# Performance work log

Measured on AMD Instinct MI355X. Metric: run time of the kernel, lower is better.

The kernel has to match this reference:

```python
import jax, jax.numpy as jnp
import numpy as np

ISIZE = 1024
OSIZE = 1024
EPS = 1e-5  # torch nn.LayerNorm default


def setup_inputs() -> dict:
    key = jax.random.key(0)
    k0, k1, k2 = jax.random.split(key, 3)
    B, S = 32, 256
    x = jax.random.normal(k0, (B, S, ISIZE), dtype=jnp.float32)
    # Linear(isize + osize, 4*osize): W stored as (in, out) for x @ W
    scale = 1.0 / np.sqrt(ISIZE + OSIZE)
    W = jax.random.uniform(k1, (ISIZE + OSIZE, 4 * OSIZE), dtype=jnp.float32,
                           minval=-scale, maxval=scale)
    b = jax.random.uniform(k2, (4 * OSIZE,), dtype=jnp.float32,
                           minval=-scale, maxval=scale)
    gamma = jnp.ones((4, OSIZE), dtype=jnp.float32)   # LayerNorm((4, osize)) weight
    beta = jnp.zeros((4, OSIZE), dtype=jnp.float32)   # LayerNorm((4, osize)) bias
    init_hx = jnp.zeros((1, OSIZE), dtype=jnp.float32)
    init_cx = jnp.zeros((1, OSIZE), dtype=jnp.float32)
    return {"x": x, "W": W, "b": b, "gamma": gamma, "beta": beta,
            "init_hx": init_hx, "init_cx": init_cx}


def _layernorm_2d(z, gamma, beta):
    # Normalize jointly over the last two dims (4, osize), per torch LayerNorm((4, osize))
    mean = jnp.mean(z, axis=(-2, -1), keepdims=True)
    var = jnp.var(z, axis=(-2, -1), keepdims=True)
    return (z - mean) * jax.lax.rsqrt(var + EPS) * gamma + beta


def reference(x, W, b, gamma, beta, init_hx, init_cx):
    B, S, _ = x.shape
    osize = init_hx.shape[-1]
    hx = jnp.broadcast_to(init_hx, (B, osize))  # prepare_initState: expand to batch
    cx = jnp.broadcast_to(init_cx, (B, osize))

    def step(carry, xt):
        h, c = carry
        comb = jnp.concatenate([xt, h], axis=-1) @ W + b       # [B, 4*osize]
        comb = _layernorm_2d(comb.reshape(B, 4, osize), gamma, beta)
        ig, fg, hidden, og = comb[:, 0], comb[:, 1], comb[:, 2], comb[:, 3]
        c = jax.nn.sigmoid(fg) * c + jax.nn.sigmoid(ig) * jnp.tanh(hidden)
        h = jax.nn.sigmoid(og) * c                              # RNMT+ cell: out = og * cell
        return (h, c), h

    xs = jnp.swapaxes(x, 0, 1)                                  # [S, B, isize]
    _, outs = jax.lax.scan(step, (hx, cx), xs)
    return jnp.swapaxes(outs, 0, 1)                             # [B, S, osize]
```

## Files before the change

kernel.cpp:

```cpp
#include <hip/hip_runtime.h>
#include <hip/hip_bf16.h>

#define NB 32
#define NS 256
#define NI 1024
#define NO 1024
#define NK 2048
#define NC 4096
#define LN_EPS 1e-5f

typedef __attribute__((ext_vector_type(4))) float f32x4;
typedef __attribute__((ext_vector_type(4))) unsigned int u32x4;

__device__ __forceinline__ f32x4 mfma_bf16_16x16x32(u32x4 a, u32x4 b, f32x4 c) {
  asm volatile("v_mfma_f32_16x16x32_bf16 %0, %1, %2, %0" : "+v"(c) : "v"(a), "v"(b));
  return c;
}

__device__ __forceinline__ float sigf(float x) { return 1.0f / (1.0f + __expf(-x)); }
__device__ __forceinline__ float tanhfast(float x) {
  return 1.0f - 2.0f / (__expf(2.0f * x) + 1.0f);
}


__global__ void pack_x(const float* __restrict__ x, __hip_bfloat16* __restrict__ xfrag) {
  const int t = blockIdx.x, kt = blockIdx.y;
  const int tid = threadIdx.x;
  const int plane = tid >> 6, l = tid & 63, q = (l >> 4), ln = l & 15;
  const int m = plane * 16 + ln;
  const float* src = x + ((size_t)m * NS + t) * NI + kt * 32 + q * 8;
  float4 v0 = *(const float4*)src;
  float4 v1 = *(const float4*)(src + 4);
  __align__(16) __hip_bfloat16 tmp[8];
  tmp[0] = __float2bfloat16(v0.x); tmp[1] = __float2bfloat16(v0.y);
  tmp[2] = __float2bfloat16(v0.z); tmp[3] = __float2bfloat16(v0.w);
  tmp[4] = __float2bfloat16(v1.x); tmp[5] = __float2bfloat16(v1.y);
  tmp[6] = __float2bfloat16(v1.z); tmp[7] = __float2bfloat16(v1.w);
  *(u32x4*)(xfrag + (((size_t)t * 32 + kt) * 2 + plane) * 512 + l * 8) = *(const u32x4*)tmp;
}

__global__ void pack_wf(const float* __restrict__ W, __hip_bfloat16* __restrict__ WF) {
  const int blk = blockIdx.x;
  const int b = blk >> 6, kt = blk & 63;
  const int l = threadIdx.x, q = l >> 4, c = l & 15;
  const int n  = ((c >> 2) << 10) + b * 4 + (c & 3);
  const int k0 = kt * 32 + q * 8;
  __align__(16) __hip_bfloat16 tmp[8];
#pragma unroll
  for (int j = 0; j < 8; ++j)
    tmp[j] = __float2bfloat16(W[(size_t)(k0 + j) * NC + n]);
  *(u32x4*)(WF + ((size_t)(b * 64 + kt) * 64 + l) * 8) = *(const u32x4*)tmp;
}

__device__ __forceinline__ size_t hfrag_idx(int m, int j) {
  const int kt = j >> 5, q = (j >> 3) & 3, jj = j & 7;
  const int plane = m >> 4, l = q * 16 + (m & 15);
  return (((size_t)kt * 2 + plane) * 64 + l) * 8 + jj;
}

__global__ void init_state(const float* __restrict__ hx0, const float* __restrict__ cx0,
                           __hip_bfloat16* __restrict__ hfrag, float* __restrict__ cst,
                           float* __restrict__ hf) {
  const int i = blockIdx.x * 256 + threadIdx.x;
  const int m = i >> 10, j = i & (NO - 1);
  const float hv = hx0[j];
  hfrag[hfrag_idx(m, j)] = __float2bfloat16(hv);
  hf[i]  = hv;
  cst[i] = cx0[j];
}

__global__ __launch_bounds__(512)
void xgemm_all(const __hip_bfloat16* __restrict__ xfrag,
               const __hip_bfloat16* __restrict__ WF,
               const float* __restrict__ bias,
               __hip_bfloat16* __restrict__ xa) {
  __shared__ __align__(16) float xch[8 * 2 * 256];
  const int b = blockIdx.x, tid = threadIdx.x;
  const int wv = tid >> 6, l = tid & 63;
  const int kt0 = wv * 4;
  u32x4 bb[4];
  {
    const __hip_bfloat16* bp = WF + ((size_t)(b * 64 + kt0) * 64 + l) * 8;
#pragma unroll
    for (int i = 0; i < 4; ++i) bb[i] = *(const u32x4*)(bp + (size_t)i * 512);
  }
  const int row = tid >> 4, c = tid & 15;
  const int p = row >> 4, rr = row & 15;
  const int idx = ((rr >> 2) * 16 + c) * 4 + (rr & 3);
  const int n = ((c >> 2) << 10) + b * 4 + (c & 3);
  const float bn = bias[n];

  for (int t = 0; t < NS; ++t) {
    f32x4 acc0 = {0.f, 0.f, 0.f, 0.f}, acc1 = {0.f, 0.f, 0.f, 0.f};
    asm volatile("s_nop 1" ::);
    const __hip_bfloat16* ap = xfrag + ((size_t)t * 32 + kt0) * 1024 + l * 8;
#pragma unroll
    for (int i = 0; i < 4; ++i) {
      u32x4 a0 = *(const u32x4*)(ap + (size_t)i * 1024);
      u32x4 a1 = *(const u32x4*)(ap + (size_t)i * 1024 + 512);
      acc0 = mfma_bf16_16x16x32(a0, bb[i], acc0);
      acc1 = mfma_bf16_16x16x32(a1, bb[i], acc1);
    }
    asm volatile("s_nop 7\n\ts_nop 7" ::);
    *(f32x4*)(xch + (wv * 2 + 0) * 256 + l * 4) = acc0;
    *(f32x4*)(xch + (wv * 2 + 1) * 256 + l * 4) = acc1;
    __syncthreads();
    float v = bn;
#pragma unroll
    for (int w = 0; w < 8; ++w) v += xch[(w * 2 + p) * 256 + idx];
    xa[((size_t)t * 256 + b) * 512 + tid] = __float2bfloat16(v);
    __syncthreads();
  }
}

__global__ __launch_bounds__(512)
void step_gemm_h(const __hip_bfloat16* __restrict__ hfrag,
                 const __hip_bfloat16* __restrict__ WF,
                 const __hip_bfloat16* __restrict__ xa,
                 float* __restrict__ comb, int t) {
  __shared__ __align__(16) float xch[8 * 2 * 256];
  const int b = blockIdx.x, tid = threadIdx.x;
  const int wv = tid >> 6, l = tid & 63;
  const int kt0 = wv * 4;
  const __hip_bfloat16* ap = hfrag + (size_t)kt0 * 1024 + l * 8;
  const __hip_bfloat16* bp = WF + ((size_t)(b * 64 + 32 + kt0) * 64 + l) * 8;

  f32x4 acc0 = {0.f, 0.f, 0.f, 0.f}, acc1 = {0.f, 0.f, 0.f, 0.f};
  asm volatile("s_nop 1" ::);
#pragma unroll
  for (int i = 0; i < 4; ++i) {
    u32x4 a0 = *(const u32x4*)(ap + (size_t)i * 1024);
    u32x4 a1 = *(const u32x4*)(ap + (size_t)i * 1024 + 512);
    u32x4 bbv = *(const u32x4*)(bp + (size_t)i * 512);
    acc0 = mfma_bf16_16x16x32(a0, bbv, acc0);
    acc1 = mfma_bf16_16x16x32(a1, bbv, acc1);
  }
  asm volatile("s_nop 7\n\ts_nop 7" ::);

  *(f32x4*)(xch + (wv * 2 + 0) * 256 + l * 4) = acc0;
  *(f32x4*)(xch + (wv * 2 + 1) * 256 + l * 4) = acc1;
  __syncthreads();

  const int row = tid >> 4, c = tid & 15;
  const int p = row >> 4, rr = row & 15;
  const int idx = ((rr >> 2) * 16 + c) * 4 + (rr & 3);
  const int n = ((c >> 2) << 10) + b * 4 + (c & 3);
  float v = __bfloat162float(xa[((size_t)t * 256 + b) * 512 + tid]);
#pragma unroll
  for (int w = 0; w < 8; ++w) v += xch[(w * 2 + p) * 256 + idx];
  comb[(size_t)row * NC + n] = v;
}

__global__ __launch_bounds__(512)
void step_gemm_mfma(const __hip_bfloat16* __restrict__ xfrag,
                    const __hip_bfloat16* __restrict__ hfrag,
                    const __hip_bfloat16* __restrict__ WF,
                    const float* __restrict__ bias,
                    float* __restrict__ comb, int t) {
  __shared__ __align__(16) float xch[8 * 2 * 256];
  const int b = blockIdx.x, tid = threadIdx.x;
  const int wv = tid >> 6, l = tid & 63;

  const __hip_bfloat16* ap = (wv < 4)
      ? xfrag + ((size_t)t * 32 + wv * 8) * 1024 + l * 8
      : hfrag + ((size_t)(wv - 4) * 8) * 1024 + l * 8;
  const __hip_bfloat16* bp = WF + ((size_t)(b * 64 + wv * 8) * 64 + l) * 8;

  f32x4 acc0 = {0.f, 0.f, 0.f, 0.f}, acc1 = {0.f, 0.f, 0.f, 0.f};
  asm volatile("s_nop 1" ::);
#pragma unroll
  for (int i = 0; i < 8; ++i) {
    u32x4 a0 = *(const u32x4*)(ap + (size_t)i * 1024);
    u32x4 a1 = *(const u32x4*)(ap + (size_t)i * 1024 + 512);
    u32x4 bb = *(const u32x4*)(bp + (size_t)i * 512);
    acc0 = mfma_bf16_16x16x32(a0, bb, acc0);
    acc1 = mfma_bf16_16x16x32(a1, bb, acc1);
  }
  asm volatile("s_nop 7\n\ts_nop 7" ::);

  *(f32x4*)(xch + (wv * 2 + 0) * 256 + l * 4) = acc0;
  *(f32x4*)(xch + (wv * 2 + 1) * 256 + l * 4) = acc1;
  __syncthreads();

  const int row = tid >> 4, c = tid & 15;
  const int p = row >> 4, rr = row & 15;
  const int idx = ((rr >> 2) * 16 + c) * 4 + (rr & 3);
  const int n = ((c >> 2) << 10) + b * 4 + (c & 3);
  float v = bias[n];
#pragma unroll
  for (int w = 0; w < 8; ++w) v += xch[(w * 2 + p) * 256 + idx];
  comb[(size_t)row * NC + n] = v;
}

__global__ __launch_bounds__(1024)
void step_update_row(const float* __restrict__ comb,
                     const float* __restrict__ gamma,
                     const float* __restrict__ beta,
                     float* __restrict__ cst,
                     float* __restrict__ out,
                     __hip_bfloat16* __restrict__ hfrag,
                     int t) {
  __shared__ __align__(16) float combL[NC];
  __shared__ float red[16][2];
  __shared__ float stat[2];
  const int m = blockIdx.x, tid = threadIdx.x;

  f32x4 cv = *(const f32x4*)(comb + (size_t)m * NC + tid * 4);
  *(f32x4*)(combL + tid * 4) = cv;
  float s  = cv[0] + cv[1] + cv[2] + cv[3];
  float ss = cv[0] * cv[0] + cv[1] * cv[1] + cv[2] * cv[2] + cv[3] * cv[3];
#pragma unroll
  for (int off = 1; off < 64; off <<= 1) {
    s  += __shfl_xor(s, off);
    ss += __shfl_xor(ss, off);
  }
  const int wid = tid >> 6;
  if ((tid & 63) == 0) { red[wid][0] = s; red[wid][1] = ss; }
  __syncthreads();
  if (tid == 0) {
    float s2 = 0.f, ss2 = 0.f;
#pragma unroll
    for (int i = 0; i < 16; ++i) { s2 += red[i][0]; ss2 += red[i][1]; }
    const float mean = s2 * (1.f / NC);
    const float var  = ss2 * (1.f / NC) - mean * mean;
    stat[0] = mean;
    stat[1] = rsqrtf(var + LN_EPS);
  }
  __syncthreads();
  const float mean = stat[0], rs = stat[1];
  const int j = tid;
  const float iv = (combL[j]          - mean) * rs * gamma[j]          + beta[j];
  const float fv = (combL[NO + j]     - mean) * rs * gamma[NO + j]     + beta[NO + j];
  const float gv = (combL[2 * NO + j] - mean) * rs * gamma[2 * NO + j] + beta[2 * NO + j];
  const float ov = (combL[3 * NO + j] - mean) * rs * gamma[3 * NO + j] + beta[3 * NO + j];
  const float cold = cst[(size_t)m * NO + j];
  const float cc = sigf(fv) * cold + sigf(iv) * tanhfast(gv);
  const float hh = sigf(ov) * cc;
  cst[(size_t)m * NO + j] = cc;
  out[((size_t)m * NS + t) * NO + j] = hh;
  hfrag[hfrag_idx(m, j)] = __float2bfloat16(hh);
}


__launch_bounds__(256)
__global__ void step_gemm_f32(const float* __restrict__ x, const float* __restrict__ hf,
                              const float* __restrict__ W, const float* __restrict__ bias,
                              float* __restrict__ comb, int t) {
  const int blk = blockIdx.x;
  const int tid = threadIdx.x;
  const int n   = blk * 16 + (tid & 15);
  const int mlo = tid >> 4;
  float a0 = 0.f, a1 = 0.f;
  for (int k = 0; k < NI; ++k) {
    const float wv = W[(size_t)k * NC + n];
    a0 += x[((size_t)mlo * NS + t) * NI + k] * wv;
    a1 += x[((size_t)(mlo + 16) * NS + t) * NI + k] * wv;
  }
  for (int k = 0; k < NO; ++k) {
    const float wv = W[(size_t)(NI + k) * NC + n];
    a0 += hf[mlo * NO + k] * wv;
    a1 += hf[(mlo + 16) * NO + k] * wv;
  }
  comb[(size_t)mlo * NC + n] = a0 + bias[n];
  comb[(size_t)(mlo + 16) * NC + n] = a1 + bias[n];
}

__global__ __launch_bounds__(1024)
void step_update_row_f32(const float* __restrict__ comb,
                         const float* __restrict__ gamma,
                         const float* __restrict__ beta,
                         float* __restrict__ cst,
                         float* __restrict__ out,
                         float* __restrict__ hf,
                         int t) {
  __shared__ __align__(16) float combL[NC];
  __shared__ float red[16][2];
  __shared__ float stat[2];
  const int m = blockIdx.x, tid = threadIdx.x;
  f32x4 cv = *(const f32x4*)(comb + (size_t)m * NC + tid * 4);
  *(f32x4*)(combL + tid * 4) = cv;
  float s  = cv[0] + cv[1] + cv[2] + cv[3];
  float ss = cv[0] * cv[0] + cv[1] * cv[1] + cv[2] * cv[2] + cv[3] * cv[3];
#pragma unroll
  for (int off = 1; off < 64; off <<= 1) {
    s  += __shfl_xor(s, off);
    ss += __shfl_xor(ss, off);
  }
  const int wid = tid >> 6;
  if ((tid & 63) == 0) { red[wid][0] = s; red[wid][1] = ss; }
  __syncthreads();
  if (tid == 0) {
    float s2 = 0.f, ss2 = 0.f;
    for (int i = 0; i < 16; ++i) { s2 += red[i][0]; ss2 += red[i][1]; }
    const float mean = s2 * (1.f / NC);
    const float var  = ss2 * (1.f / NC) - mean * mean;
    stat[0] = mean;
    stat[1] = rsqrtf(var + LN_EPS);
  }
  __syncthreads();
  const float mean = stat[0], rs = stat[1];
  const int j = tid;
  const float iv = (combL[j]          - mean) * rs * gamma[j]          + beta[j];
  const float fv = (combL[NO + j]     - mean) * rs * gamma[NO + j]     + beta[NO + j];
  const float gv = (combL[2 * NO + j] - mean) * rs * gamma[2 * NO + j] + beta[2 * NO + j];
  const float ov = (combL[3 * NO + j] - mean) * rs * gamma[3 * NO + j] + beta[3 * NO + j];
  const float cold = cst[(size_t)m * NO + j];
  const float cc = sigf(fv) * cold + sigf(iv) * tanhfast(gv);
  const float hh = sigf(ov) * cc;
  cst[(size_t)m * NO + j] = cc;
  out[((size_t)m * NS + t) * NO + j] = hh;
  hf[(size_t)m * NO + j] = hh;
}


extern "C" void kernel_launch(void* const* d_in, const int* in_sizes, int n_in,
                              void* d_out, int out_size, void* d_ws, size_t ws_size,
                              hipStream_t stream) {
  (void)in_sizes; (void)n_in; (void)out_size;
  const float* x     = (const float*)d_in[0];
  const float* W     = (const float*)d_in[1];
  const float* bias  = (const float*)d_in[2];
  const float* gamma = (const float*)d_in[3];
  const float* beta  = (const float*)d_in[4];
  const float* hx0   = (const float*)d_in[5];
  const float* cx0   = (const float*)d_in[6];
  float* outp = (float*)d_out;

  char* ws = (char*)d_ws;
  size_t off = 0;
  auto alloc = [&](size_t bytes) -> char* {
    off = (off + 255) & ~(size_t)255;
    char* p = ws + off;
    off += bytes;
    return p;
  };
  float* comb           = (float*)alloc((size_t)NB * NC * 4);
  float* cst            = (float*)alloc((size_t)NB * NO * 4);
  float* hf             = (float*)alloc((size_t)NB * NO * 4);
  __hip_bfloat16* hfrag = (__hip_bfloat16*)alloc((size_t)NB * NO * 2);
  __hip_bfloat16* xfrag = (__hip_bfloat16*)alloc((size_t)NB * NS * NI * 2);
  __hip_bfloat16* WF    = (__hip_bfloat16*)alloc((size_t)NK * NC * 2);
  const size_t off_tier2 = off;
  __hip_bfloat16* xa    = (__hip_bfloat16*)alloc((size_t)NS * NB * NC * 2);
  const size_t off_tier1 = off;

  const bool tier1 = (ws_size >= off_tier1);
  const bool tier2 = (ws_size >= off_tier2);

  if (tier1) {
    hipLaunchKernelGGL(init_state, dim3((NB * NO) / 256), dim3(256), 0, stream,
                       hx0, cx0, hfrag, cst, hf);
    hipLaunchKernelGGL(pack_x, dim3(NS, 32), dim3(128), 0, stream, x, xfrag);
    hipLaunchKernelGGL(pack_wf, dim3(256 * 64), dim3(64), 0, stream, W, WF);
    hipLaunchKernelGGL(xgemm_all, dim3(256), dim3(512), 0, stream,
                       xfrag, WF, bias, xa);
    for (int t = 0; t < NS; ++t) {
      hipLaunchKernelGGL(step_gemm_h, dim3(256), dim3(512), 0, stream,
                         hfrag, WF, xa, comb, t);
      hipLaunchKernelGGL(step_update_row, dim3(NB), dim3(1024), 0, stream,
                         comb, gamma, beta, cst, outp, hfrag, t);
    }
  } else if (tier2) {
    hipLaunchKernelGGL(init_state, dim3((NB * NO) / 256), dim3(256), 0, stream,
                       hx0, cx0, hfrag, cst, hf);
    hipLaunchKernelGGL(pack_x, dim3(NS, 32), dim3(128), 0, stream, x, xfrag);
    hipLaunchKernelGGL(pack_wf, dim3(256 * 64), dim3(64), 0, stream, W, WF);
    for (int t = 0; t < NS; ++t) {
      hipLaunchKernelGGL(step_gemm_mfma, dim3(256), dim3(512), 0, stream,
                         xfrag, hfrag, WF, bias, comb, t);
      hipLaunchKernelGGL(step_update_row, dim3(NB), dim3(1024), 0, stream,
                         comb, gamma, beta, cst, outp, hfrag, t);
    }
  } else {
    hipLaunchKernelGGL(init_state, dim3((NB * NO) / 256), dim3(256), 0, stream,
                       hx0, cx0, hfrag, cst, hf);
    for (int t = 0; t < NS; ++t) {
      hipLaunchKernelGGL(step_gemm_f32, dim3(256), dim3(256), 0, stream,
                         x, hf, W, bias, comb, t);
      hipLaunchKernelGGL(step_update_row_f32, dim3(NB), dim3(1024), 0, stream,
                         comb, gamma, beta, cst, outp, hf, t);
    }
  }
}
```

Before: 2.497 ms.

## Fuse per-step h-GEMM and LayerNorm/LSTM update via atomic grid barrier

Merges the per-timestep recurrent GEMM and the row-wise LayerNorm plus gate update into one kernel, so each step needs one launch instead of two. Row sum and sum-of-squares are accumulated with coherent float atomics into per-step slots. An atomic counter acts as a grid-wide barrier before each block normalises and updates its own columns. This removes a launch and the round trip of the comb buffer through global memory. In exchange it assumes all 256 blocks are co-resident, and it takes variance as E[x^2]-mean^2 in fp32, which is less numerically stable.

```diff
diff --git a/kernel.cpp b/kernel.cpp
--- a/kernel.cpp
+++ b/kernel.cpp
@@ -8,6 +8,10 @@
 #define NK 2048
 #define NC 4096
 #define LN_EPS 1e-5f
+#define SPIN_GUARD (1 << 18)
+
+#define SROW_STRIDE 16
+#define CNT_STRIDE  32
 
 typedef __attribute__((ext_vector_type(4))) float f32x4;
 typedef __attribute__((ext_vector_type(4))) unsigned int u32x4;
@@ -20,6 +24,30 @@
 __device__ __forceinline__ float sigf(float x) { return 1.0f / (1.0f + __expf(-x)); }
 __device__ __forceinline__ float tanhfast(float x) {
   return 1.0f - 2.0f / (__expf(2.0f * x) + 1.0f);
+}
+
+__device__ __forceinline__ unsigned int load_coh_u32(const void* p) {
+  unsigned int v;
+  asm volatile("global_load_dword %0, %1, off sc0 sc1\n\ts_waitcnt vmcnt(0)"
+               : "=&v"(v) : "v"(p));
+  return v;
+}
+#define COH_LOAD2_F32(d0, d1, a0, a1)                                   \
+  asm volatile("global_load_dword %0, %2, off sc0 sc1\n\t"              \
+               "global_load_dword %1, %3, off sc0 sc1\n\t"              \
+               "s_waitcnt vmcnt(0)"                                     \
+               : "=&v"(d0), "=&v"(d1) : "v"(a0), "v"(a1))
+__device__ __forceinline__ void atomic_add_coh_u32(void* p, unsigned int v) {
+  asm volatile("global_atomic_add %0, %1, off sc1" :: "v"(p), "v"(v) : "memory");
+}
+__device__ __forceinline__ void atomic_add_coh_f32(void* p, float v) {
+  asm volatile("global_atomic_add_f32 %0, %1, off sc1" :: "v"(p), "v"(v) : "memory");
+}
+__device__ __forceinline__ void poll_coh_ge(const unsigned int* p, unsigned int target) {
+  for (int g = 0; g < SPIN_GUARD; ++g) {
+    if (load_coh_u32(p) >= target) return;
+    __builtin_amdgcn_s_sleep(2);
+  }
 }
 
 
@@ -114,16 +142,25 @@
 }
 
 __global__ __launch_bounds__(512)
-void step_gemm_h(const __hip_bfloat16* __restrict__ hfrag,
-                 const __hip_bfloat16* __restrict__ WF,
-                 const __hip_bfloat16* __restrict__ xa,
-                 float* __restrict__ comb, int t) {
+void step_fused(__hip_bfloat16* hfrag,
+                const __hip_bfloat16* __restrict__ WF,
+                const __hip_bfloat16* __restrict__ xa,
+                const float* __restrict__ gamma,
+                const float* __restrict__ beta,
+                float* __restrict__ cst,
+                float* __restrict__ out,
+                float* __restrict__ srow_t,
+                unsigned int* __restrict__ scnt_t,
+                int t) {
   __shared__ __align__(16) float xch[8 * 2 * 256];
+  __shared__ __align__(16) float combB[32 * 16];
   const int b = blockIdx.x, tid = threadIdx.x;
   const int wv = tid >> 6, l = tid & 63;
+
   const int kt0 = wv * 4;
   const __hip_bfloat16* ap = hfrag + (size_t)kt0 * 1024 + l * 8;
   const __hip_bfloat16* bp = WF + ((size_t)(b * 64 + 32 + kt0) * 64 + l) * 8;
+  const float xav = __bfloat162float(xa[((size_t)t * 256 + b) * 512 + tid]);
 
   f32x4 acc0 = {0.f, 0.f, 0.f, 0.f}, acc1 = {0.f, 0.f, 0.f, 0.f};
   asm volatile("s_nop 1" ::);
@@ -142,13 +179,65 @@
   __syncthreads();
 
   const int row = tid >> 4, c = tid & 15;
-  const int p = row >> 4, rr = row & 15;
-  const int idx = ((rr >> 2) * 16 + c) * 4 + (rr & 3);
-  const int n = ((c >> 2) << 10) + b * 4 + (c & 3);
-  float v = __bfloat162float(xa[((size_t)t * 256 + b) * 512 + tid]);
-#pragma unroll
-  for (int w = 0; w < 8; ++w) v += xch[(w * 2 + p) * 256 + idx];
-  comb[(size_t)row * NC + n] = v;
+  {
+    const int p = row >> 4, rr = row & 15;
+    const int idx = ((rr >> 2) * 16 + c) * 4 + (rr & 3);
+    float v = xav;
+#pragma unroll
+    for (int w = 0; w < 8; ++w) v += xch[(w * 2 + p) * 256 + idx];
+    combB[row * 16 + c] = v;
+    float s = v, ss = v * v;
+#pragma unroll
+    for (int off = 1; off < 16; off <<= 1) {
+      s  += __shfl_xor(s, off);
+      ss += __shfl_xor(ss, off);
+    }
+    if (c == 0) {
+      float* slot = srow_t + row * SROW_STRIDE;
+      atomic_add_coh_f32(slot + 0, s);
+      atomic_add_coh_f32(slot + 8, ss);
+    }
+  }
+  asm volatile("s_waitcnt vmcnt(0)" ::: "memory");
+  __syncthreads();
+  if (tid == 0) {
+    atomic_add_coh_u32(scnt_t, 1u);
+    poll_coh_ge(scnt_t, 256u);
+  }
+  __syncthreads();
+
+  if (wv == 0) {
+    const int gm = l >> 1, gh = l & 1;
+    const int j0 = b * 4 + 2 * gh;
+    const float* slot = srow_t + gm * SROW_STRIDE;
+    float sv, ssv;
+    COH_LOAD2_F32(sv, ssv, slot + 0, slot + 8);
+    const float mean = sv * (1.f / NC);
+    const float var  = ssv * (1.f / NC) - mean * mean;
+    const float rs = rsqrtf(var + LN_EPS);
+    const int cb = 2 * gh;
+    float pre[4][2];
+#pragma unroll
+    for (int g = 0; g < 4; ++g) {
+      const float ga0 = gamma[g * NO + j0], ga1 = gamma[g * NO + j0 + 1];
+      const float be0 = beta[g * NO + j0],  be1 = beta[g * NO + j0 + 1];
+      pre[g][0] = (combB[gm * 16 + g * 4 + cb]     - mean) * rs * ga0 + be0;
+      pre[g][1] = (combB[gm * 16 + g * 4 + cb + 1] - mean) * rs * ga1 + be1;
+    }
+    float2 cold = *(const float2*)(cst + (size_t)gm * NO + j0);
+    const float cc0 = sigf(pre[1][0]) * cold.x + sigf(pre[0][0]) * tanhfast(pre[2][0]);
+    const float cc1 = sigf(pre[1][1]) * cold.y + sigf(pre[0][1]) * tanhfast(pre[2][1]);
+    const float hh0 = sigf(pre[3][0]) * cc0;
+    const float hh1 = sigf(pre[3][1]) * cc1;
+    float2 cnew; cnew.x = cc0; cnew.y = cc1;
+    *(float2*)(cst + (size_t)gm * NO + j0) = cnew;
+    float2 o2; o2.x = hh0; o2.y = hh1;
+    *(float2*)(out + ((size_t)gm * NS + t) * NO + j0) = o2;
+    __hip_bfloat16 hb0 = __float2bfloat16(hh0), hb1 = __float2bfloat16(hh1);
+    unsigned int hp = (unsigned int)*(unsigned short*)&hb0 |
+                      ((unsigned int)*(unsigned short*)&hb1 << 16);
+    *(unsigned int*)(hfrag + hfrag_idx(gm, j0)) = hp;
+  }
 }
 
 __global__ __launch_bounds__(512)
@@ -338,6 +427,8 @@
   float* cst            = (float*)alloc((size_t)NB * NO * 4);
   float* hf             = (float*)alloc((size_t)NB * NO * 4);
   __hip_bfloat16* hfrag = (__hip_bfloat16*)alloc((size_t)NB * NO * 2);
+  float* srow           = (float*)alloc((size_t)NS * 32 * SROW_STRIDE * 4);
+  unsigned int* scnt    = (unsigned int*)alloc((size_t)NS * CNT_STRIDE * 4);
   __hip_bfloat16* xfrag = (__hip_bfloat16*)alloc((size_t)NB * NS * NI * 2);
   __hip_bfloat16* WF    = (__hip_bfloat16*)alloc((size_t)NK * NC * 2);
   const size_t off_tier2 = off;
@@ -348,6 +439,8 @@
   const bool tier2 = (ws_size >= off_tier2);
 
   if (tier1) {
+    hipMemsetAsync(srow, 0, (size_t)NS * 32 * SROW_STRIDE * 4, stream);
+    hipMemsetAsync(scnt, 0, (size_t)NS * CNT_STRIDE * 4, stream);
     hipLaunchKernelGGL(init_state, dim3((NB * NO) / 256), dim3(256), 0, stream,
                        hx0, cx0, hfrag, cst, hf);
     hipLaunchKernelGGL(pack_x, dim3(NS, 32), dim3(128), 0, stream, x, xfrag);
@@ -355,10 +448,10 @@
     hipLaunchKernelGGL(xgemm_all, dim3(256), dim3(512), 0, stream,
                        xfrag, WF, bias, xa);
     for (int t = 0; t < NS; ++t) {
-      hipLaunchKernelGGL(step_gemm_h, dim3(256), dim3(512), 0, stream,
-                         hfrag, WF, xa, comb, t);
-      hipLaunchKernelGGL(step_update_row, dim3(NB), dim3(1024), 0, stream,
-                         comb, gamma, beta, cst, outp, hfrag, t);
+      hipLaunchKernelGGL(step_fused, dim3(256), dim3(512), 0, stream,
+                         hfrag, WF, xa, gamma, beta, cst, outp,
+                         srow + (size_t)t * 32 * SROW_STRIDE,
+                         scnt + (size_t)t * CNT_STRIDE, t);
     }
   } else if (tier2) {
     hipLaunchKernelGGL(init_state, dim3((NB * NO) / 256), dim3(256), 0, stream,
```

New measurement: 6.150 ms. +146.3%, slower.
